# Performance work log

Measured on AMD Instinct MI355X. Metric: run time of the kernel, lower is better.

Reference implementation:

```python
import jax, jax.numpy as jnp
import numpy as np

N = 20000          # nodes
E = 320000         # edges (avg degree 16)
FS = 1000          # feature_size (resnet feature width)
IN = 250 + FS + 250 + 85 * 3  # 1755, actual concat width


def setup_inputs() -> dict:
    key = jax.random.key(0)
    ks = jax.random.split(key, 16)
    # structured node feature matrix x: [layer_id | resnet(1000) | rel_size | rgb(3)]
    layer = jax.random.randint(ks[0], (N, 1), 1, 4).astype(jnp.float32)      # {1,2,3}
    resnet = jax.random.normal(ks[1], (N, FS), jnp.float32)
    rel = jax.random.uniform(ks[2], (N, 1), jnp.float32)                      # [0,1] -> idx 0..10
    colors = jax.random.randint(ks[3], (N, 3), 0, 256).astype(jnp.float32)
    x = jnp.concatenate([layer, resnet, rel, colors], axis=1)  # [N,1005]
    edge_index = jax.random.randint(ks[4], (2, E), 0, N)
    edge_attr = jax.random.uniform(ks[5], (E,), jnp.float32)

    def lin(k, fi, fo):
        return jax.random.normal(k, (fi, fo), jnp.float32) / np.sqrt(fi).astype(np.float32)

    return {
        "x": x,
        "edge_index": edge_index,
        "edge_attr": edge_attr,
        "layer_table": jax.random.normal(ks[6], (3, 250), jnp.float32),
        "rel_table": jax.random.normal(ks[7], (11, 250), jnp.float32),
        "color_table": jax.random.normal(ks[8], (256, 85), jnp.float32),
        "W1": lin(ks[9], IN, 512), "b1": jnp.zeros((512,), jnp.float32),
        "W2": lin(ks[10], 512, 256), "b2": jnp.zeros((256,), jnp.float32),
        "W3": lin(ks[11], 256, 64), "b3": jnp.zeros((64,), jnp.float32),
        "Wp": lin(ks[12], 64, 3), "bp": jnp.zeros((3,), jnp.float32),
    }


def _gcn_conv(h, src, dst, ew, W, b):
    # PyG GCNConv: h' = D^{-1/2} (A + I) D^{-1/2} (h W) + b, with edge weights ew
    h = h @ W
    deg = jax.ops.segment_sum(ew, dst, num_segments=N) + 1.0  # +1 for self-loop weight
    dinv = jnp.where(deg > 0.0, jax.lax.rsqrt(deg), 0.0)
    norm = dinv[src] * ew * dinv[dst]                          # [E]
    agg = jax.ops.segment_sum(h[src] * norm[:, None], dst, num_segments=N)
    agg = agg + h * (dinv * dinv)[:, None]                     # self-loop term
    return agg + b


def reference(x, edge_index, edge_attr, layer_table, rel_table, color_table,
              W1, b1, W2, b2, W3, b3, Wp, bp):
    src, dst = edge_index[0], edge_index[1]
    li = (x[:, 0] - 1.0).astype(jnp.int32)                      # layer id 0..2
    le = layer_table[li]                                        # [N,250]
    resnet = x[:, 1:FS + 1]                                     # [N,1000]
    ri = jnp.round(jnp.abs(x[:, FS + 1]) * 10.0).astype(jnp.int32)
    re = rel_table[ri]                                          # [N,250]
    ci = x[:, -3:].astype(jnp.int32)
    ce = color_table[ci].reshape(x.shape[0], -1)                # [N,255]
    h = jnp.concatenate([le, resnet, re, ce], axis=1)           # [N,1755]

    lrelu = lambda v: jax.nn.leaky_relu(v, 0.01)
    h = lrelu(_gcn_conv(h, src, dst, edge_attr, W1, b1))
    h = lrelu(_gcn_conv(h, src, dst, edge_attr, W2, b2))
    h = lrelu(_gcn_conv(h, src, dst, edge_attr, W3, b3))
    return h @ Wp + bp                                          # [N,3]
```

## Files before the change

### kernel.cpp

```cpp
#include <hip/hip_runtime.h>
#include <hip/hip_bf16.h>

#define NNODES 20000
#define NEDGES 320000
#define XW 1005
#define MP 20096

typedef __attribute__((ext_vector_type(8))) short short8;
typedef __attribute__((ext_vector_type(4))) float f32x4;
typedef __attribute__((ext_vector_type(4))) unsigned short u16x4;

typedef const __attribute__((address_space(1))) unsigned int gas_u32;
typedef __attribute__((address_space(3))) unsigned int las_u32;

__device__ inline void ld16(const unsigned short* g, unsigned short* l) {
    __builtin_amdgcn_global_load_lds((gas_u32*)g, (las_u32*)l, 16, 0, 0);
}

__device__ inline void split1(float v, unsigned short& h, unsigned short& l) {
    unsigned u = __float_as_uint(v);
    h = (unsigned short)(u >> 16);
    float hf = __uint_as_float(u & 0xffff0000u);
    l = (unsigned short)(__float_as_uint(v - hf) >> 16);
}


__global__ void edge_deg_kernel(const int* __restrict__ ei, const float* __restrict__ ea,
                                float* __restrict__ deg, int* __restrict__ counts, int E) {
    int e = blockIdx.x * 256 + threadIdx.x;
    if (e >= E) return;
    int dst = ei[E + e];
    atomicAdd(&deg[dst], ea[e]);
    atomicAdd(&counts[dst], 1);
}

__global__ void dinv_kernel(const float* __restrict__ deg, float* __restrict__ dinv, int n) {
    int i = blockIdx.x * 256 + threadIdx.x;
    if (i >= n) return;
    float d = deg[i] + 1.0f;
    dinv[i] = 1.0f / sqrtf(d);
}

__global__ __launch_bounds__(1024) void scan_kernel(const int* __restrict__ counts,
                                                    int* __restrict__ offs, int n) {
    __shared__ int wsum[16];
    __shared__ int wpre[16];
    __shared__ int carry_s;
    int t = threadIdx.x;
    int lane = t & 63, wid = t >> 6;
    if (t == 0) carry_s = 0;
    __syncthreads();
    for (int base = 0; base < n; base += 1024) {
        int i = base + t;
        int v = (i < n) ? counts[i] : 0;
        int x = v;
#pragma unroll
        for (int d = 1; d < 64; d <<= 1) {
            int u = __shfl_up(x, d, 64);
            if (lane >= d) x += u;
        }
        if (lane == 63) wsum[wid] = x;
        __syncthreads();
        if (wid == 0) {
            int s = (lane < 16) ? wsum[lane] : 0;
#pragma unroll
            for (int d = 1; d < 16; d <<= 1) {
                int u = __shfl_up(s, d, 64);
                if (lane >= d) s += u;
            }
            if (lane < 16) wpre[lane] = s;
        }
        __syncthreads();
        int carry = carry_s;
        int prefix = carry + (wid > 0 ? wpre[wid - 1] : 0);
        if (i < n) offs[i] = prefix + x - v;
        __syncthreads();
        if (t == 1023) carry_s = prefix + x;
    }
    __syncthreads();
    if (t == 0) offs[n] = carry_s;
}

__global__ void scatter_kernel(const int* __restrict__ ei, const float* __restrict__ ea,
                               const float* __restrict__ dinv, const int* __restrict__ offs,
                               int* __restrict__ cursor, int* __restrict__ csr_src,
                               float* __restrict__ csr_norm, int E) {
    int e = blockIdx.x * 256 + threadIdx.x;
    if (e >= E) return;
    int src = ei[e];
    int dst = ei[E + e];
    int slot = offs[dst] + atomicAdd(&cursor[dst], 1);
    csr_src[slot] = src;
    csr_norm[slot] = dinv[src] * ea[e] * dinv[dst];
}


__global__ void idx_kernel(const float* __restrict__ x, int* __restrict__ idx8, int n) {
    int i = blockIdx.x * 256 + threadIdx.x;
    if (i >= n) return;
    const float* r = x + (size_t)i * XW;
    idx8[i * 8 + 0] = (int)(r[0] - 1.0f);
    idx8[i * 8 + 1] = (int)rintf(fabsf(r[1001]) * 10.0f);
    idx8[i * 8 + 2] = (int)r[1002];
    idx8[i * 8 + 3] = (int)r[1003];
    idx8[i * 8 + 4] = (int)r[1004];
}


__global__ __launch_bounds__(256) void tables_kernel(
    const float* __restrict__ layer_table, const float* __restrict__ rel_table,
    const float* __restrict__ color_table, const float* __restrict__ W1,
    float* __restrict__ T) {
    int g = blockIdx.x * 256 + threadIdx.x;
    if (g >= 782 * 512) return;
    int row = g >> 9, col = g & 511;
    float acc = 0.0f;
    if (row < 3) {
        for (int k = 0; k < 250; ++k)
            acc += layer_table[row * 250 + k] * W1[(size_t)k * 512 + col];
    } else if (row < 14) {
        int r = row - 3;
        for (int k = 0; k < 250; ++k)
            acc += rel_table[r * 250 + k] * W1[(size_t)(1250 + k) * 512 + col];
    } else {
        int r = row - 14;
        int j = r >> 8, v = r & 255;
        int base = 1500 + 85 * j;
        for (int k = 0; k < 85; ++k)
            acc += color_table[v * 85 + k] * W1[(size_t)(base + k) * 512 + col];
    }
    T[(size_t)row * 512 + col] = acc;
}


__global__ __launch_bounds__(256) void a1_split_kernel(const float* __restrict__ x,
                                                       unsigned short* __restrict__ Ah,
                                                       unsigned short* __restrict__ Al) {
    int g = blockIdx.x * 256 + threadIdx.x;
    if (g >= NNODES * 256) return;
    int row = g >> 8, c4 = (g & 255) << 2;
    const float* xp = x + (size_t)row * XW + 1 + c4;
    u16x4 h, l;
#pragma unroll
    for (int i = 0; i < 4; ++i) {
        float v = (c4 + i < 1000) ? xp[i] : 0.0f;
        unsigned short hh, ll;
        split1(v, hh, ll);
        h[i] = (short)hh; l[i] = (short)ll;
    }
    *(u16x4*)&Ah[(size_t)row * 1024 + c4] = h;
    *(u16x4*)&Al[(size_t)row * 1024 + c4] = l;
}

__global__ __launch_bounds__(256) void bt_split_kernel(const float* __restrict__ W, int ldw,
                                                       int koff, int K, int Kp, int Ncols,
                                                       unsigned short* __restrict__ Bh,
                                                       unsigned short* __restrict__ Bl) {
    int g = blockIdx.x * 256 + threadIdx.x;
    int kp4 = Kp >> 2;
    if (g >= Ncols * kp4) return;
    int n = g / kp4, c4 = (g % kp4) << 2;
    u16x4 h, l;
#pragma unroll
    for (int i = 0; i < 4; ++i) {
        int k = c4 + i;
        float v = (k < K) ? W[(size_t)(koff + k) * ldw + n] : 0.0f;
        unsigned short hh, ll;
        split1(v, hh, ll);
        h[i] = (short)hh; l[i] = (short)ll;
    }
    *(u16x4*)&Bh[(size_t)n * Kp + c4] = h;
    *(u16x4*)&Bl[(size_t)n * Kp + c4] = l;
}


template <int BN, bool EMB>
__global__ __launch_bounds__(256, 3) void gemm_split_kernel(
    const unsigned short* __restrict__ Ah, const unsigned short* __restrict__ Al, int Kp,
    const unsigned short* __restrict__ Bh, const unsigned short* __restrict__ Bl,
    float* __restrict__ C, int ldc, int M,
    const float* __restrict__ T, const int* __restrict__ idx8) {
    constexpr int NT = BN / 32;
    constexpr int BJ = BN / 64;
    __shared__ __align__(16) unsigned short sAh[128 * 32];
    __shared__ __align__(16) unsigned short sAl[128 * 32];
    __shared__ __align__(16) unsigned short sBh[BN * 32];
    __shared__ __align__(16) unsigned short sBl[BN * 32];

    const int t = threadIdx.x;
    const int lane = t & 63;
    const int w = t >> 6;
    const int wr = w >> 1, wc = w & 1;
    const int l15 = lane & 15, quad = lane >> 4;
    const int row0 = blockIdx.y * 128;
    const int col0 = blockIdx.x * BN;

    const int si_r = lane >> 2;
    const int si_s = lane & 3;
    const int schunk = si_s ^ ((si_r >> 1) & 3);
    const int sw = (quad ^ ((l15 >> 1) & 3)) * 8;

    const unsigned short* gAh[2]; const unsigned short* gAl[2];
    unsigned short* dAh[2]; unsigned short* dAl[2];
#pragma unroll
    for (int j = 0; j < 2; ++j) {
        int ra = w * 32 + j * 16 + si_r;
        size_t e = (size_t)(row0 + ra) * Kp + schunk * 8;
        gAh[j] = Ah + e; gAl[j] = Al + e;
        dAh[j] = &sAh[(w * 32 + j * 16) * 32];
        dAl[j] = &sAl[(w * 32 + j * 16) * 32];
    }
    const unsigned short* gBh[BJ]; const unsigned short* gBl[BJ];
    unsigned short* dBh[BJ]; unsigned short* dBl[BJ];
#pragma unroll
    for (int j = 0; j < BJ; ++j) {
        int rb = w * (BN / 4) + j * 16 + si_r;
        size_t e = (size_t)(col0 + rb) * Kp + schunk * 8;
        gBh[j] = Bh + e; gBl[j] = Bl + e;
        dBh[j] = &sBh[(w * (BN / 4) + j * 16) * 32];
        dBl[j] = &sBl[(w * (BN / 4) + j * 16) * 32];
    }

    f32x4 acc[4][NT];
#pragma unroll
    for (int i = 0; i < 4; ++i)
#pragma unroll
        for (int j = 0; j < NT; ++j)
            acc[i][j] = (f32x4){0.f, 0.f, 0.f, 0.f};

    for (int kb = 0; kb < Kp; kb += 32) {
#pragma unroll
        for (int j = 0; j < 2; ++j) {
            ld16(gAh[j] + kb, dAh[j]);
            ld16(gAl[j] + kb, dAl[j]);
        }
#pragma unroll
        for (int j = 0; j < BJ; ++j) {
            ld16(gBh[j] + kb, dBh[j]);
            ld16(gBl[j] + kb, dBl[j]);
        }
        __syncthreads();

        short8 fah[4], fal[4], fbh[NT], fbl[NT];
#pragma unroll
        for (int mt = 0; mt < 4; ++mt) {
            int off = (wr * 64 + mt * 16 + l15) * 32 + sw;
            fah[mt] = *(const short8*)&sAh[off];
            fal[mt] = *(const short8*)&sAl[off];
        }
#pragma unroll
        for (int nt = 0; nt < NT; ++nt) {
            int off = (wc * (BN / 2) + nt * 16 + l15) * 32 + sw;
            fbh[nt] = *(const short8*)&sBh[off];
            fbl[nt] = *(const short8*)&sBl[off];
        }
#pragma unroll
        for (int mt = 0; mt < 4; ++mt)
#pragma unroll
            for (int nt = 0; nt < NT; ++nt)
                acc[mt][nt] = __builtin_amdgcn_mfma_f32_16x16x32_bf16(fah[mt], fbh[nt], acc[mt][nt], 0, 0, 0);
#pragma unroll
        for (int mt = 0; mt < 4; ++mt)
#pragma unroll
            for (int nt = 0; nt < NT; ++nt)
                acc[mt][nt] = __builtin_amdgcn_mfma_f32_16x16x32_bf16(fah[mt], fbl[nt], acc[mt][nt], 0, 0, 0);
#pragma unroll
        for (int mt = 0; mt < 4; ++mt)
#pragma unroll
            for (int nt = 0; nt < NT; ++nt)
                acc[mt][nt] = __builtin_amdgcn_mfma_f32_16x16x32_bf16(fal[mt], fbh[nt], acc[mt][nt], 0, 0, 0);
        __syncthreads();
    }

#pragma unroll
    for (int mt = 0; mt < 4; ++mt)
#pragma unroll
        for (int r = 0; r < 4; ++r) {
            int row = row0 + wr * 64 + mt * 16 + quad * 4 + r;
            if (row >= M) continue;
            if (EMB) {
                const int* ix = idx8 + row * 8;
                const float* t0 = T + (size_t)ix[0] * 512;
                const float* t1 = T + (size_t)(3 + ix[1]) * 512;
                const float* t2 = T + (size_t)(14 + ix[2]) * 512;
                const float* t3 = T + (size_t)(270 + ix[3]) * 512;
                const float* t4 = T + (size_t)(526 + ix[4]) * 512;
#pragma unroll
                for (int nt = 0; nt < NT; ++nt) {
                    int col = col0 + wc * (BN / 2) + nt * 16 + l15;
                    float e = t0[col] + t1[col] + t2[col] + t3[col] + t4[col];
                    C[(size_t)row * ldc + col] = acc[mt][nt][r] + e;
                }
            } else {
#pragma unroll
                for (int nt = 0; nt < NT; ++nt) {
                    int col = col0 + wc * (BN / 2) + nt * 16 + l15;
                    C[(size_t)row * ldc + col] = acc[mt][nt][r];
                }
            }
        }
}


template <int F, int CW, bool SPLIT>
__global__ __launch_bounds__(256) void agg_cols_kernel(
    const float* __restrict__ H, const float* __restrict__ dinv,
    const int* __restrict__ offs, const int* __restrict__ csr_src,
    const float* __restrict__ csr_norm, const float* __restrict__ bias,
    float* __restrict__ outf, unsigned short* __restrict__ Hh,
    unsigned short* __restrict__ Hl, int n_nodes) {
    constexpr int LPN = CW / 4;
    constexpr int NPB = 256 / LPN;
    constexpr int NCH = F / CW;
    constexpr int ECAP = 2048;
    __shared__ int   se[ECAP];
    __shared__ float sn[ECAP];

    const int chunk = blockIdx.x & (NCH - 1);
    const int nb    = blockIdx.x / NCH;
    const int n0 = nb * NPB;
    const int n1 = min(n0 + NPB, n_nodes);
    if (n0 >= n_nodes) return;

    const int estart = offs[n0];
    const int eend   = offs[n1];
    const int ecnt   = eend - estart;
    const bool inlds = (ecnt <= ECAP);
    if (inlds) {
        for (int i = threadIdx.x; i < ecnt; i += 256) {
            se[i] = csr_src[estart + i];
            sn[i] = csr_norm[estart + i];
        }
    }
    __syncthreads();

    const int n = n0 + threadIdx.x / LPN;
    if (n >= n_nodes) return;
    const int lane = threadIdx.x % LPN;
    const int c = chunk * CW + lane * 4;

    float di = dinv[n];
    float s = di * di;
    float4 h = *(const float4*)(H + (size_t)n * F + c);
    float4 acc = make_float4(h.x * s, h.y * s, h.z * s, h.w * s);
    int e0 = offs[n], e1 = offs[n + 1];
    if (inlds) {
        for (int e = e0 - estart; e < e1 - estart; ++e) {
            int src = se[e];
            float w = sn[e];
            float4 v = *(const float4*)(H + (size_t)src * F + c);
            acc.x += v.x * w; acc.y += v.y * w; acc.z += v.z * w; acc.w += v.w * w;
        }
    } else {
        for (int e = e0; e < e1; ++e) {
            int src = csr_src[e];
            float w = csr_norm[e];
            float4 v = *(const float4*)(H + (size_t)src * F + c);
            acc.x += v.x * w; acc.y += v.y * w; acc.z += v.z * w; acc.w += v.w * w;
        }
    }
    float4 b = *(const float4*)(bias + c);
    acc.x += b.x; acc.y += b.y; acc.z += b.z; acc.w += b.w;
    acc.x = acc.x > 0.f ? acc.x : 0.01f * acc.x;
    acc.y = acc.y > 0.f ? acc.y : 0.01f * acc.y;
    acc.z = acc.z > 0.f ? acc.z : 0.01f * acc.z;
    acc.w = acc.w > 0.f ? acc.w : 0.01f * acc.w;
    if (SPLIT) {
        u16x4 hh, ll;
        unsigned short a, bb;
        split1(acc.x, a, bb); hh[0] = (short)a; ll[0] = (short)bb;
        split1(acc.y, a, bb); hh[1] = (short)a; ll[1] = (short)bb;
        split1(acc.z, a, bb); hh[2] = (short)a; ll[2] = (short)bb;
        split1(acc.w, a, bb); hh[3] = (short)a; ll[3] = (short)bb;
        *(u16x4*)(Hh + (size_t)n * F + c) = hh;
        *(u16x4*)(Hl + (size_t)n * F + c) = ll;
    } else {
        *(float4*)(outf + (size_t)n * F + c) = acc;
    }
}


__global__ void proj_kernel(const float* __restrict__ H, const float* __restrict__ Wp,
                            const float* __restrict__ bp, float* __restrict__ out, int n_nodes) {
    int t = blockIdx.x * 192 + threadIdx.x;
    int n = t / 3, j = t % 3;
    if (n >= n_nodes) return;
    float acc = bp[j];
    const float* h = H + (size_t)n * 64;
    for (int c = 0; c < 64; ++c) acc += h[c] * Wp[c * 3 + j];
    out[n * 3 + j] = acc;
}


static inline size_t aln(size_t v) { return (v + 255) & ~(size_t)255; }

extern "C" void kernel_launch(void* const* d_in, const int* in_sizes, int n_in,
                              void* d_out, int out_size, void* d_ws, size_t ws_size,
                              hipStream_t stream) {
    const float* x           = (const float*)d_in[0];
    const int*   edge_index  = (const int*)d_in[1];
    const float* edge_attr   = (const float*)d_in[2];
    const float* layer_table = (const float*)d_in[3];
    const float* rel_table   = (const float*)d_in[4];
    const float* color_table = (const float*)d_in[5];
    const float* W1 = (const float*)d_in[6];
    const float* b1 = (const float*)d_in[7];
    const float* W2 = (const float*)d_in[8];
    const float* b2 = (const float*)d_in[9];
    const float* W3 = (const float*)d_in[10];
    const float* b3 = (const float*)d_in[11];
    const float* Wp = (const float*)d_in[12];
    const float* bp = (const float*)d_in[13];
    float* out = (float*)d_out;

    const int N = NNODES, E = NEDGES;

    char* p = (char*)d_ws;
    float* deg      = (float*)p; p += aln((size_t)N * 4);
    float* dinv     = (float*)p; p += aln((size_t)N * 4);
    float* T        = (float*)p; p += aln((size_t)782 * 512 * 4);
    float* csr_norm = (float*)p; p += aln((size_t)E * 4);
    float* C        = (float*)p; p += aln((size_t)MP * 512 * 4);
    unsigned short* BIG = (unsigned short*)p; p += aln((size_t)MP * 2048 * 2);
    unsigned short* Bt1h = (unsigned short*)p; p += aln((size_t)512 * 1024 * 2);
    unsigned short* Bt1l = (unsigned short*)p; p += aln((size_t)512 * 1024 * 2);
    unsigned short* Bt2h = (unsigned short*)p; p += aln((size_t)256 * 512 * 2);
    unsigned short* Bt2l = (unsigned short*)p; p += aln((size_t)256 * 512 * 2);
    unsigned short* Bt3h = (unsigned short*)p; p += aln((size_t)64 * 256 * 2);
    unsigned short* Bt3l = (unsigned short*)p; p += aln((size_t)64 * 256 * 2);
    int*   counts   = (int*)p;   p += aln((size_t)N * 4);
    int*   cursor   = (int*)p;   p += aln((size_t)N * 4);
    int*   csr_src  = (int*)p;   p += aln((size_t)E * 4);
    int*   idx8     = (int*)p;   p += aln((size_t)N * 8 * 4);
    int*   offs     = (int*)p;   p += aln((size_t)(N + 1) * 4);

    unsigned short* A1h = BIG;
    unsigned short* A1l = BIG + (size_t)MP * 1024;
    unsigned short* H2h = BIG;
    unsigned short* H2l = BIG + (size_t)MP * 512;
    unsigned short* H3h = BIG + (size_t)MP * 1024;
    unsigned short* H3l = BIG + (size_t)MP * 1024 + (size_t)MP * 256;
    float*          H4  = (float*)(BIG + (size_t)MP * 1536);

    hipMemsetAsync(deg, 0, (size_t)N * 4, stream);
    hipMemsetAsync(counts, 0, (size_t)N * 4, stream);
    hipMemsetAsync(cursor, 0, (size_t)N * 4, stream);

    edge_deg_kernel<<<(E + 255) / 256, 256, 0, stream>>>(edge_index, edge_attr, deg, counts, E);
    dinv_kernel<<<(N + 255) / 256, 256, 0, stream>>>(deg, dinv, N);
    scan_kernel<<<1, 1024, 0, stream>>>(counts, offs, N);
    scatter_kernel<<<(E + 255) / 256, 256, 0, stream>>>(edge_index, edge_attr, dinv, offs,
                                                        cursor, csr_src, csr_norm, E);
    idx_kernel<<<(N + 255) / 256, 256, 0, stream>>>(x, idx8, N);
    tables_kernel<<<(782 * 512 + 255) / 256, 256, 0, stream>>>(layer_table, rel_table,
                                                               color_table, W1, T);
    a1_split_kernel<<<(NNODES * 256) / 256, 256, 0, stream>>>(x, A1h, A1l);
    bt_split_kernel<<<(512 * 256 + 255) / 256, 256, 0, stream>>>(W1, 512, 250, 1000, 1024, 512, Bt1h, Bt1l);
    bt_split_kernel<<<(256 * 128 + 255) / 256, 256, 0, stream>>>(W2, 256, 0, 512, 512, 256, Bt2h, Bt2l);
    bt_split_kernel<<<(64 * 64 + 255) / 256, 256, 0, stream>>>(W3, 64, 0, 256, 256, 64, Bt3h, Bt3l);

    const int nrb = MP / 128;

    {
        dim3 grid(512 / 128, nrb);
        gemm_split_kernel<128, true><<<grid, 256, 0, stream>>>(A1h, A1l, 1024, Bt1h, Bt1l,
                                                               C, 512, N, T, idx8);
        int nblocks = (N + 15) / 16;
        agg_cols_kernel<512, 64, true><<<8 * nblocks, 256, 0, stream>>>(
            C, dinv, offs, csr_src, csr_norm, b1, nullptr, H2h, H2l, N);
    }
    {
        dim3 grid(256 / 128, nrb);
        gemm_split_kernel<128, false><<<grid, 256, 0, stream>>>(H2h, H2l, 512, Bt2h, Bt2l,
                                                                C, 256, N, nullptr, nullptr);
        int nblocks = (N + 31) / 32;
        agg_cols_kernel<256, 32, true><<<8 * nblocks, 256, 0, stream>>>(
            C, dinv, offs, csr_src, csr_norm, b2, nullptr, H3h, H3l, N);
    }
    {
        dim3 grid(1, nrb);
        gemm_split_kernel<64, false><<<grid, 256, 0, stream>>>(H3h, H3l, 256, Bt3h, Bt3l,
                                                               C, 64, N, nullptr, nullptr);
        int nblocks = (N + 63) / 64;
        agg_cols_kernel<64, 16, false><<<4 * nblocks, 256, 0, stream>>>(
            C, dinv, offs, csr_src, csr_norm, b3, H4, nullptr, nullptr, N);
    }
    proj_kernel<<<(N * 3 + 191) / 192, 192, 0, stream>>>(H4, Wp, bp, out, N);
}
```

Baseline: 503.0 us.

## Fuse prep kernels, parallelize scan, shrink GEMM row tile with XCD-aware mapping

```diff
diff --git a/kernel.cpp b/kernel.cpp
--- a/kernel.cpp
+++ b/kernel.cpp
@@ -24,61 +24,173 @@
     l = (unsigned short)(__float_as_uint(v - hf) >> 16);
 }
 
-
-__global__ void edge_deg_kernel(const int* __restrict__ ei, const float* __restrict__ ea,
-                                float* __restrict__ deg, int* __restrict__ counts, int E) {
-    int e = blockIdx.x * 256 + threadIdx.x;
-    if (e >= E) return;
-    int dst = ei[E + e];
-    atomicAdd(&deg[dst], ea[e]);
-    atomicAdd(&counts[dst], 1);
-}
-
-__global__ void dinv_kernel(const float* __restrict__ deg, float* __restrict__ dinv, int n) {
-    int i = blockIdx.x * 256 + threadIdx.x;
-    if (i >= n) return;
-    float d = deg[i] + 1.0f;
-    dinv[i] = 1.0f / sqrtf(d);
-}
-
-__global__ __launch_bounds__(1024) void scan_kernel(const int* __restrict__ counts,
-                                                    int* __restrict__ offs, int n) {
-    __shared__ int wsum[16];
-    __shared__ int wpre[16];
-    __shared__ int carry_s;
-    int t = threadIdx.x;
-    int lane = t & 63, wid = t >> 6;
-    if (t == 0) carry_s = 0;
-    __syncthreads();
-    for (int base = 0; base < n; base += 1024) {
-        int i = base + t;
+#define PB_EDGE  1250
+#define PB_IDX   1329
+#define PB_A1    21329
+#define PB_BT1   21841
+#define PB_BT2   21969
+#define PB_BT3   21985
+#define PB_TAB   23549
+
+__device__ inline void bt_split_body(int g, const float* __restrict__ W, int ldw,
+                                     int koff, int K, int Kp, int Ncols,
+                                     unsigned short* __restrict__ Bh,
+                                     unsigned short* __restrict__ Bl) {
+    int kp4 = Kp >> 2;
+    if (g >= Ncols * kp4) return;
+    int n = g / kp4, c4 = (g % kp4) << 2;
+    u16x4 h, l;
+#pragma unroll
+    for (int i = 0; i < 4; ++i) {
+        int k = c4 + i;
+        float v = (k < K) ? W[(size_t)(koff + k) * ldw + n] : 0.0f;
+        unsigned short hh, ll;
+        split1(v, hh, ll);
+        h[i] = (short)hh; l[i] = (short)ll;
+    }
+    *(u16x4*)&Bh[(size_t)n * Kp + c4] = h;
+    *(u16x4*)&Bl[(size_t)n * Kp + c4] = l;
+}
+
+__global__ __launch_bounds__(256) void prep_kernel(
+    const float* __restrict__ x, const int* __restrict__ ei, const float* __restrict__ ea,
+    const float* __restrict__ layer_table, const float* __restrict__ rel_table,
+    const float* __restrict__ color_table,
+    const float* __restrict__ W1, const float* __restrict__ W2, const float* __restrict__ W3,
+    float* __restrict__ deg, int* __restrict__ counts, int* __restrict__ idx8,
+    unsigned short* __restrict__ A1h, unsigned short* __restrict__ A1l,
+    unsigned short* __restrict__ Bt1h, unsigned short* __restrict__ Bt1l,
+    unsigned short* __restrict__ Bt2h, unsigned short* __restrict__ Bt2l,
+    unsigned short* __restrict__ Bt3h, unsigned short* __restrict__ Bt3l,
+    float* __restrict__ T) {
+    const int b = blockIdx.x;
+    const int t = threadIdx.x;
+    if (b < PB_EDGE) {
+        int e = b * 256 + t;
+        if (e >= NEDGES) return;
+        int dst = ei[NEDGES + e];
+        atomicAdd(&deg[dst], ea[e]);
+        atomicAdd(&counts[dst], 1);
+    } else if (b < PB_IDX) {
+        int i = (b - PB_EDGE) * 256 + t;
+        if (i >= NNODES) return;
+        const float* r = x + (size_t)i * XW;
+        idx8[i * 8 + 0] = (int)(r[0] - 1.0f);
+        idx8[i * 8 + 1] = (int)rintf(fabsf(r[1001]) * 10.0f);
+        idx8[i * 8 + 2] = (int)r[1002];
+        idx8[i * 8 + 3] = (int)r[1003];
+        idx8[i * 8 + 4] = (int)r[1004];
+    } else if (b < PB_A1) {
+        int row = b - PB_IDX;
+        int c4 = t << 2;
+        const float* xp = x + (size_t)row * XW + 1 + c4;
+        u16x4 h, l;
+#pragma unroll
+        for (int i = 0; i < 4; ++i) {
+            float v = (c4 + i < 1000) ? xp[i] : 0.0f;
+            unsigned short hh, ll;
+            split1(v, hh, ll);
+            h[i] = (short)hh; l[i] = (short)ll;
+        }
+        *(u16x4*)&A1h[(size_t)row * 1024 + c4] = h;
+        *(u16x4*)&A1l[(size_t)row * 1024 + c4] = l;
+    } else if (b < PB_BT1) {
+        bt_split_body((b - PB_A1) * 256 + t, W1, 512, 250, 1000, 1024, 512, Bt1h, Bt1l);
+    } else if (b < PB_BT2) {
+        bt_split_body((b - PB_BT1) * 256 + t, W2, 256, 0, 512, 512, 256, Bt2h, Bt2l);
+    } else if (b < PB_BT3) {
+        bt_split_body((b - PB_BT2) * 256 + t, W3, 64, 0, 256, 256, 64, Bt3h, Bt3l);
+    } else {
+        int g = (b - PB_BT3) * 256 + t;
+        if (g >= 782 * 512) return;
+        int row = g >> 9, col = g & 511;
+        float acc = 0.0f;
+        if (row < 3) {
+            for (int k = 0; k < 250; ++k)
+                acc += layer_table[row * 250 + k] * W1[(size_t)k * 512 + col];
+        } else if (row < 14) {
+            int r = row - 3;
+            for (int k = 0; k < 250; ++k)
+                acc += rel_table[r * 250 + k] * W1[(size_t)(1250 + k) * 512 + col];
+        } else {
+            int r = row - 14;
+            int j = r >> 8, v = r & 255;
+            int base = 1500 + 85 * j;
+            for (int k = 0; k < 85; ++k)
+                acc += color_table[v * 85 + k] * W1[(size_t)(base + k) * 512 + col];
+        }
+        T[(size_t)row * 512 + col] = acc;
+    }
+}
+
+
+__global__ __launch_bounds__(1024) void scan_p1_kernel(const int* __restrict__ counts,
+                                                       int* __restrict__ bsum,
+                                                       const float* __restrict__ deg,
+                                                       float* __restrict__ dinv, int n) {
+    int b = blockIdx.x;
+    if (b < 20) {
+        __shared__ int ws[16];
+        int t = threadIdx.x, lane = t & 63, wid = t >> 6;
+        int i = b * 1024 + t;
         int v = (i < n) ? counts[i] : 0;
-        int x = v;
-#pragma unroll
-        for (int d = 1; d < 64; d <<= 1) {
-            int u = __shfl_up(x, d, 64);
-            if (lane >= d) x += u;
-        }
-        if (lane == 63) wsum[wid] = x;
+#pragma unroll
+        for (int d = 32; d; d >>= 1) v += __shfl_down(v, d, 64);
+        if (lane == 0) ws[wid] = v;
         __syncthreads();
         if (wid == 0) {
-            int s = (lane < 16) ? wsum[lane] : 0;
-#pragma unroll
-            for (int d = 1; d < 16; d <<= 1) {
-                int u = __shfl_up(s, d, 64);
-                if (lane >= d) s += u;
-            }
-            if (lane < 16) wpre[lane] = s;
-        }
-        __syncthreads();
-        int carry = carry_s;
-        int prefix = carry + (wid > 0 ? wpre[wid - 1] : 0);
-        if (i < n) offs[i] = prefix + x - v;
-        __syncthreads();
-        if (t == 1023) carry_s = prefix + x;
-    }
+            int s = (lane < 16) ? ws[lane] : 0;
+#pragma unroll
+            for (int d = 8; d; d >>= 1) s += __shfl_down(s, d, 64);
+            if (lane == 0) bsum[b] = s;
+        }
+    } else {
+        int i = (b - 20) * 1024 + threadIdx.x;
+        if (i < n) { float d = deg[i] + 1.0f; dinv[i] = 1.0f / sqrtf(d); }
+    }
+}
+
+__global__ void scan_p2_kernel(const int* __restrict__ bsum, int* __restrict__ boffs,
+                               int* __restrict__ offs, int n, int nb) {
+    int lane = threadIdx.x;
+    int v = (lane < nb) ? bsum[lane] : 0;
+    int xv = v;
+#pragma unroll
+    for (int d = 1; d < 64; d <<= 1) {
+        int u = __shfl_up(xv, d, 64);
+        if (lane >= d) xv += u;
+    }
+    if (lane < nb) boffs[lane] = xv - v;
+    if (lane == nb - 1) offs[n] = xv;
+}
+
+__global__ __launch_bounds__(1024) void scan_p3_kernel(const int* __restrict__ counts,
+                                                       const int* __restrict__ boffs,
+                                                       int* __restrict__ offs, int n) {
+    __shared__ int wsum[16], wpre[16];
+    int t = threadIdx.x, lane = t & 63, wid = t >> 6;
+    int i = blockIdx.x * 1024 + t;
+    int v = (i < n) ? counts[i] : 0;
+    int xv = v;
+#pragma unroll
+    for (int d = 1; d < 64; d <<= 1) {
+        int u = __shfl_up(xv, d, 64);
+        if (lane >= d) xv += u;
+    }
+    if (lane == 63) wsum[wid] = xv;
     __syncthreads();
-    if (t == 0) offs[n] = carry_s;
+    if (wid == 0) {
+        int s = (lane < 16) ? wsum[lane] : 0;
+#pragma unroll
+        for (int d = 1; d < 16; d <<= 1) {
+            int u = __shfl_up(s, d, 64);
+            if (lane >= d) s += u;
+        }
+        if (lane < 16) wpre[lane] = s;
+    }
+    __syncthreads();
+    int prefix = boffs[blockIdx.x] + (wid > 0 ? wpre[wid - 1] : 0);
+    if (i < n) offs[i] = prefix + xv - v;
 }
 
 __global__ void scatter_kernel(const int* __restrict__ ei, const float* __restrict__ ea,
@@ -95,95 +207,16 @@
 }
 
 
-__global__ void idx_kernel(const float* __restrict__ x, int* __restrict__ idx8, int n) {
-    int i = blockIdx.x * 256 + threadIdx.x;
-    if (i >= n) return;
-    const float* r = x + (size_t)i * XW;
-    idx8[i * 8 + 0] = (int)(r[0] - 1.0f);
-    idx8[i * 8 + 1] = (int)rintf(fabsf(r[1001]) * 10.0f);
-    idx8[i * 8 + 2] = (int)r[1002];
-    idx8[i * 8 + 3] = (int)r[1003];
-    idx8[i * 8 + 4] = (int)r[1004];
-}
-
-
-__global__ __launch_bounds__(256) void tables_kernel(
-    const float* __restrict__ layer_table, const float* __restrict__ rel_table,
-    const float* __restrict__ color_table, const float* __restrict__ W1,
-    float* __restrict__ T) {
-    int g = blockIdx.x * 256 + threadIdx.x;
-    if (g >= 782 * 512) return;
-    int row = g >> 9, col = g & 511;
-    float acc = 0.0f;
-    if (row < 3) {
-        for (int k = 0; k < 250; ++k)
-            acc += layer_table[row * 250 + k] * W1[(size_t)k * 512 + col];
-    } else if (row < 14) {
-        int r = row - 3;
-        for (int k = 0; k < 250; ++k)
-            acc += rel_table[r * 250 + k] * W1[(size_t)(1250 + k) * 512 + col];
-    } else {
-        int r = row - 14;
-        int j = r >> 8, v = r & 255;
-        int base = 1500 + 85 * j;
-        for (int k = 0; k < 85; ++k)
-            acc += color_table[v * 85 + k] * W1[(size_t)(base + k) * 512 + col];
-    }
-    T[(size_t)row * 512 + col] = acc;
-}
-
-
-__global__ __launch_bounds__(256) void a1_split_kernel(const float* __restrict__ x,
-                                                       unsigned short* __restrict__ Ah,
-                                                       unsigned short* __restrict__ Al) {
-    int g = blockIdx.x * 256 + threadIdx.x;
-    if (g >= NNODES * 256) return;
-    int row = g >> 8, c4 = (g & 255) << 2;
-    const float* xp = x + (size_t)row * XW + 1 + c4;
-    u16x4 h, l;
-#pragma unroll
-    for (int i = 0; i < 4; ++i) {
-        float v = (c4 + i < 1000) ? xp[i] : 0.0f;
-        unsigned short hh, ll;
-        split1(v, hh, ll);
-        h[i] = (short)hh; l[i] = (short)ll;
-    }
-    *(u16x4*)&Ah[(size_t)row * 1024 + c4] = h;
-    *(u16x4*)&Al[(size_t)row * 1024 + c4] = l;
-}
-
-__global__ __launch_bounds__(256) void bt_split_kernel(const float* __restrict__ W, int ldw,
-                                                       int koff, int K, int Kp, int Ncols,
-                                                       unsigned short* __restrict__ Bh,
-                                                       unsigned short* __restrict__ Bl) {
-    int g = blockIdx.x * 256 + threadIdx.x;
-    int kp4 = Kp >> 2;
-    if (g >= Ncols * kp4) return;
-    int n = g / kp4, c4 = (g % kp4) << 2;
-    u16x4 h, l;
-#pragma unroll
-    for (int i = 0; i < 4; ++i) {
-        int k = c4 + i;
-        float v = (k < K) ? W[(size_t)(koff + k) * ldw + n] : 0.0f;
-        unsigned short hh, ll;
-        split1(v, hh, ll);
-        h[i] = (short)hh; l[i] = (short)ll;
-    }
-    *(u16x4*)&Bh[(size_t)n * Kp + c4] = h;
-    *(u16x4*)&Bl[(size_t)n * Kp + c4] = l;
-}
-
-
-template <int BN, bool EMB>
-__global__ __launch_bounds__(256, 3) void gemm_split_kernel(
+template <int BN, int NCB, bool EMB>
+__global__ __launch_bounds__(256, 4) void gemm_split_kernel(
     const unsigned short* __restrict__ Ah, const unsigned short* __restrict__ Al, int Kp,
     const unsigned short* __restrict__ Bh, const unsigned short* __restrict__ Bl,
     float* __restrict__ C, int ldc, int M,
     const float* __restrict__ T, const int* __restrict__ idx8) {
     constexpr int NT = BN / 32;
     constexpr int BJ = BN / 64;
-    __shared__ __align__(16) unsigned short sAh[128 * 32];
-    __shared__ __align__(16) unsigned short sAl[128 * 32];
+    __shared__ __align__(16) unsigned short sAh[64 * 32];
+    __shared__ __align__(16) unsigned short sAl[64 * 32];
     __shared__ __align__(16) unsigned short sBh[BN * 32];
     __shared__ __align__(16) unsigned short sBl[BN * 32];
 
@@ -192,23 +225,27 @@
     const int w = t >> 6;
     const int wr = w >> 1, wc = w & 1;
     const int l15 = lane & 15, quad = lane >> 4;
-    const int row0 = blockIdx.y * 128;
-    const int col0 = blockIdx.x * BN;
+
+    const int total = gridDim.x;
+    const int per = total >> 3;
+    const int bid = blockIdx.x;
+    const int tile = (bid < (per << 3)) ? ((bid & 7) * per + (bid >> 3)) : bid;
+    const int row0 = (tile / NCB) * 64;
+    const int col0 = (tile % NCB) * BN;
 
     const int si_r = lane >> 2;
     const int si_s = lane & 3;
     const int schunk = si_s ^ ((si_r >> 1) & 3);
     const int sw = (quad ^ ((l15 >> 1) & 3)) * 8;
 
-    const unsigned short* gAh[2]; const unsigned short* gAl[2];
-    unsigned short* dAh[2]; unsigned short* dAl[2];
-#pragma unroll
-    for (int j = 0; j < 2; ++j) {
-        int ra = w * 32 + j * 16 + si_r;
+    const unsigned short* gAh; const unsigned short* gAl;
+    unsigned short* dAh; unsigned short* dAl;
+    {
+        int ra = w * 16 + si_r;
         size_t e = (size_t)(row0 + ra) * Kp + schunk * 8;
-        gAh[j] = Ah + e; gAl[j] = Al + e;
-        dAh[j] = &sAh[(w * 32 + j * 16) * 32];
-        dAl[j] = &sAl[(w * 32 + j * 16) * 32];
+        gAh = Ah + e; gAl = Al + e;
+        dAh = &sAh[(w * 16) * 32];
+        dAl = &sAl[(w * 16) * 32];
     }
     const unsigned short* gBh[BJ]; const unsigned short* gBl[BJ];
     unsigned short* dBh[BJ]; unsigned short* dBl[BJ];
@@ -221,19 +258,16 @@
         dBl[j] = &sBl[(w * (BN / 4) + j * 16) * 32];
     }
 
-    f32x4 acc[4][NT];
-#pragma unroll
-    for (int i = 0; i < 4; ++i)
+    f32x4 acc[2][NT];
+#pragma unroll
+    for (int i = 0; i < 2; ++i)
 #pragma unroll
         for (int j = 0; j < NT; ++j)
             acc[i][j] = (f32x4){0.f, 0.f, 0.f, 0.f};
 
     for (int kb = 0; kb < Kp; kb += 32) {
-#pragma unroll
-        for (int j = 0; j < 2; ++j) {
-            ld16(gAh[j] + kb, dAh[j]);
-            ld16(gAl[j] + kb, dAl[j]);
-        }
+        ld16(gAh + kb, dAh);
+        ld16(gAl + kb, dAl);
 #pragma unroll
         for (int j = 0; j < BJ; ++j) {
             ld16(gBh[j] + kb, dBh[j]);
@@ -241,10 +275,10 @@
         }
         __syncthreads();
 
-        short8 fah[4], fal[4], fbh[NT], fbl[NT];
-#pragma unroll
-        for (int mt = 0; mt < 4; ++mt) {
-            int off = (wr * 64 + mt * 16 + l15) * 32 + sw;
+        short8 fah[2], fal[2], fbh[NT], fbl[NT];
+#pragma unroll
+        for (int mt = 0; mt < 2; ++mt) {
+            int off = (wr * 32 + mt * 16 + l15) * 32 + sw;
             fah[mt] = *(const short8*)&sAh[off];
             fal[mt] = *(const short8*)&sAl[off];
         }
@@ -255,17 +289,17 @@
             fbl[nt] = *(const short8*)&sBl[off];
         }
 #pragma unroll
-        for (int mt = 0; mt < 4; ++mt)
+        for (int mt = 0; mt < 2; ++mt)
 #pragma unroll
             for (int nt = 0; nt < NT; ++nt)
                 acc[mt][nt] = __builtin_amdgcn_mfma_f32_16x16x32_bf16(fah[mt], fbh[nt], acc[mt][nt], 0, 0, 0);
 #pragma unroll
-        for (int mt = 0; mt < 4; ++mt)
+        for (int mt = 0; mt < 2; ++mt)
 #pragma unroll
             for (int nt = 0; nt < NT; ++nt)
                 acc[mt][nt] = __builtin_amdgcn_mfma_f32_16x16x32_bf16(fah[mt], fbl[nt], acc[mt][nt], 0, 0, 0);
 #pragma unroll
-        for (int mt = 0; mt < 4; ++mt)
+        for (int mt = 0; mt < 2; ++mt)
 #pragma unroll
             for (int nt = 0; nt < NT; ++nt)
                 acc[mt][nt] = __builtin_amdgcn_mfma_f32_16x16x32_bf16(fal[mt], fbh[nt], acc[mt][nt], 0, 0, 0);
@@ -273,10 +307,10 @@
     }
 
 #pragma unroll
-    for (int mt = 0; mt < 4; ++mt)
+    for (int mt = 0; mt < 2; ++mt)
 #pragma unroll
         for (int r = 0; r < 4; ++r) {
-            int row = row0 + wr * 64 + mt * 16 + quad * 4 + r;
+            int row = row0 + wr * 32 + mt * 16 + quad * 4 + r;
             if (row >= M) continue;
             if (EMB) {
                 const int* ix = idx8 + row * 8;
@@ -416,7 +450,9 @@
     const int N = NNODES, E = NEDGES;
 
     char* p = (char*)d_ws;
-    float* deg      = (float*)p; p += aln((size_t)N * 4);
+    float* deg      = (float*)p;
+    int*   counts   = (int*)(p + (size_t)N * 4);
+    int*   cursor   = (int*)(p + (size_t)N * 8);     p += aln((size_t)N * 12);
     float* dinv     = (float*)p; p += aln((size_t)N * 4);
     float* T        = (float*)p; p += aln((size_t)782 * 512 * 4);
     float* csr_norm = (float*)p; p += aln((size_t)E * 4);
@@ -428,11 +464,11 @@
     unsigned short* Bt2l = (unsigned short*)p; p += aln((size_t)256 * 512 * 2);
     unsigned short* Bt3h = (unsigned short*)p; p += aln((size_t)64 * 256 * 2);
     unsigned short* Bt3l = (unsigned short*)p; p += aln((size_t)64 * 256 * 2);
-    int*   counts   = (int*)p;   p += aln((size_t)N * 4);
-    int*   cursor   = (int*)p;   p += aln((size_t)N * 4);
     int*   csr_src  = (int*)p;   p += aln((size_t)E * 4);
     int*   idx8     = (int*)p;   p += aln((size_t)N * 8 * 4);
     int*   offs     = (int*)p;   p += aln((size_t)(N + 1) * 4);
+    int*   bsum     = (int*)p;   p += aln((size_t)32 * 4);
+    int*   boffs    = (int*)p;   p += aln((size_t)32 * 4);
 
     unsigned short* A1h = BIG;
     unsigned short* A1l = BIG + (size_t)MP * 1024;
@@ -442,45 +478,38 @@
     unsigned short* H3l = BIG + (size_t)MP * 1024 + (size_t)MP * 256;
     float*          H4  = (float*)(BIG + (size_t)MP * 1536);
 
-    hipMemsetAsync(deg, 0, (size_t)N * 4, stream);
-    hipMemsetAsync(counts, 0, (size_t)N * 4, stream);
-    hipMemsetAsync(cursor, 0, (size_t)N * 4, stream);
-
-    edge_deg_kernel<<<(E + 255) / 256, 256, 0, stream>>>(edge_index, edge_attr, deg, counts, E);
-    dinv_kernel<<<(N + 255) / 256, 256, 0, stream>>>(deg, dinv, N);
-    scan_kernel<<<1, 1024, 0, stream>>>(counts, offs, N);
+    hipMemsetAsync(deg, 0, (size_t)N * 12, stream);
+
+    prep_kernel<<<PB_TAB, 256, 0, stream>>>(
+        x, edge_index, edge_attr, layer_table, rel_table, color_table,
+        W1, W2, W3, deg, counts, idx8,
+        A1h, A1l, Bt1h, Bt1l, Bt2h, Bt2l, Bt3h, Bt3l, T);
+
+    scan_p1_kernel<<<40, 1024, 0, stream>>>(counts, bsum, deg, dinv, N);
+    scan_p2_kernel<<<1, 64, 0, stream>>>(bsum, boffs, offs, N, 20);
+    scan_p3_kernel<<<20, 1024, 0, stream>>>(counts, boffs, offs, N);
     scatter_kernel<<<(E + 255) / 256, 256, 0, stream>>>(edge_index, edge_attr, dinv, offs,
                                                         cursor, csr_src, csr_norm, E);
-    idx_kernel<<<(N + 255) / 256, 256, 0, stream>>>(x, idx8, N);
-    tables_kernel<<<(782 * 512 + 255) / 256, 256, 0, stream>>>(layer_table, rel_table,
-                                                               color_table, W1, T);
-    a1_split_kernel<<<(NNODES * 256) / 256, 256, 0, stream>>>(x, A1h, A1l);
-    bt_split_kernel<<<(512 * 256 + 255) / 256, 256, 0, stream>>>(W1, 512, 250, 1000, 1024, 512, Bt1h, Bt1l);
-    bt_split_kernel<<<(256 * 128 + 255) / 256, 256, 0, stream>>>(W2, 256, 0, 512, 512, 256, Bt2h, Bt2l);
-    bt_split_kernel<<<(64 * 64 + 255) / 256, 256, 0, stream>>>(W3, 64, 0, 256, 256, 64, Bt3h, Bt3l);
-
-    const int nrb = MP / 128;
+
+    const int nrb = MP / 64;
 
     {
-        dim3 grid(512 / 128, nrb);
-        gemm_split_kernel<128, true><<<grid, 256, 0, stream>>>(A1h, A1l, 1024, Bt1h, Bt1l,
-                                                               C, 512, N, T, idx8);
+        gemm_split_kernel<128, 4, true><<<nrb * 4, 256, 0, stream>>>(
+            A1h, A1l, 1024, Bt1h, Bt1l, C, 512, N, T, idx8);
         int nblocks = (N + 15) / 16;
         agg_cols_kernel<512, 64, true><<<8 * nblocks, 256, 0, stream>>>(
             C, dinv, offs, csr_src, csr_norm, b1, nullptr, H2h, H2l, N);
     }
     {
-        dim3 grid(256 / 128, nrb);
-        gemm_split_kernel<128, false><<<grid, 256, 0, stream>>>(H2h, H2l, 512, Bt2h, Bt2l,
-                                                                C, 256, N, nullptr, nullptr);
+        gemm_split_kernel<128, 2, false><<<nrb * 2, 256, 0, stream>>>(
+            H2h, H2l, 512, Bt2h, Bt2l, C, 256, N, nullptr, nullptr);
         int nblocks = (N + 31) / 32;
         agg_cols_kernel<256, 32, true><<<8 * nblocks, 256, 0, stream>>>(
             C, dinv, offs, csr_src, csr_norm, b2, nullptr, H3h, H3l, N);
     }
     {
-        dim3 grid(1, nrb);
-        gemm_split_kernel<64, false><<<grid, 256, 0, stream>>>(H3h, H3l, 256, Bt3h, Bt3l,
-                                                               C, 64, N, nullptr, nullptr);
+        gemm_split_kernel<64, 1, false><<<nrb, 256, 0, stream>>>(
+            H3h, H3l, 256, Bt3h, Bt3l, C, 64, N, nullptr, nullptr);
         int nblocks = (N + 63) / 64;
         agg_cols_kernel<64, 16, false><<<4 * nblocks, 256, 0, stream>>>(
             C, dinv, offs, csr_src, csr_norm, b3, H4, nullptr, nullptr, N);
```

Result: faster. 455.5 us (-9.4%).
